# Kernel tuning notes

Hardware: AMD Instinct MI355X
Metric: run time of the kernel (lower is better)

The kernel has to match this reference:

```python
import jax, jax.numpy as jnp
import numpy as np

N, E = 50000, 600000
H, ED = 128, 64
LN_EPS = 1e-5


def _ln(x, g, b):
    mu = jnp.mean(x, axis=-1, keepdims=True)
    var = jnp.mean(jnp.square(x - mu), axis=-1, keepdims=True)
    return (x - mu) * jax.lax.rsqrt(var + LN_EPS) * g + b


def setup_inputs() -> dict:
    key = jax.random.key(0)
    ks = jax.random.split(key, 20)
    p = lambda k, shp: (jax.random.normal(k, shp, dtype=jnp.float32) * 0.02)
    return {
        "x": jax.random.normal(ks[0], (N, H), dtype=jnp.float32),
        "edge_src": jax.random.randint(ks[1], (E,), 0, N, dtype=jnp.int32),
        "edge_dst": jax.random.randint(ks[2], (E,), 0, N, dtype=jnp.int32),
        "edge_emb": jax.random.normal(ks[3], (E, ED), dtype=jnp.float32),
        "ln1_g": jnp.ones((H,), jnp.float32), "ln1_b": jnp.zeros((H,), jnp.float32),
        "W_self": p(ks[4], (H, H)), "b_self": jnp.zeros((H,), jnp.float32),
        "W_m1": p(ks[5], (H + ED, H)), "b_m1": jnp.zeros((H,), jnp.float32),
        "W_m2": p(ks[6], (H, H)), "b_m2": jnp.zeros((H,), jnp.float32),
        "W_g1": p(ks[7], (2 * H + ED, H)), "b_g1": jnp.zeros((H,), jnp.float32),
        "W_g2": p(ks[8], (H, 1)), "b_g2": jnp.zeros((1,), jnp.float32),
        "W_agg": p(ks[9], (H, H)), "b_agg": jnp.zeros((H,), jnp.float32),
        "ln2_g": jnp.ones((H,), jnp.float32), "ln2_b": jnp.zeros((H,), jnp.float32),
        "W_f1": p(ks[10], (H, 2 * H)), "b_f1": jnp.zeros((2 * H,), jnp.float32),
        "W_f2": p(ks[11], (2 * H, H)), "b_f2": jnp.zeros((H,), jnp.float32),
    }


def reference(x, edge_src, edge_dst, edge_emb,
              ln1_g, ln1_b, W_self, b_self,
              W_m1, b_m1, W_m2, b_m2,
              W_g1, b_g1, W_g2, b_g2,
              W_agg, b_agg, ln2_g, ln2_b,
              W_f1, b_f1, W_f2, b_f2):
    n = x.shape[0]
    h = _ln(x, ln1_g, ln1_b)                      # [N,H]
    hs = h[edge_src]                              # [E,H] gather
    hd = h[edge_dst]                              # [E,H] gather
    # message MLP on [h_src || e]
    m_in = jnp.concatenate([hs, edge_emb], axis=-1)            # [E,H+ED]
    msg = jax.nn.gelu(m_in @ W_m1 + b_m1, approximate=False) @ W_m2 + b_m2
    # gate MLP on [h_dst || h_src || e]
    g_in = jnp.concatenate([hd, hs, edge_emb], axis=-1)        # [E,2H+ED]
    gate = jax.nn.sigmoid(jax.nn.gelu(g_in @ W_g1 + b_g1, approximate=False) @ W_g2 + b_g2)
    edge_repr = gate * msg                                     # [E,H]
    # scatter-mean aggregate to destination nodes
    agg = jax.ops.segment_sum(edge_repr, edge_dst, num_segments=n)   # [N,H]
    deg = jax.ops.segment_sum(jnp.ones((edge_dst.shape[0], 1), x.dtype),
                              edge_dst, num_segments=n)              # [N,1]
    agg = agg / jnp.maximum(deg, 1.0)
    update = (h @ W_self + b_self) + (agg @ W_agg + b_agg)
    out = x + update                                           # residual
    ffn_in = _ln(out, ln2_g, ln2_b)
    ffn_up = jax.nn.gelu(ffn_in @ W_f1 + b_f1, approximate=False) @ W_f2 + b_f2
    out = out + ffn_up                                         # residual
    return (out, edge_repr)
```

## Files before the change

### kernel.cpp

```cpp
#include <hip/hip_runtime.h>
#include <math.h>

#define N_NODES 50000
#define N_EDGES 600000

typedef __attribute__((ext_vector_type(8))) short bf16x8;
typedef __attribute__((ext_vector_type(4))) float f32x4;

__device__ __forceinline__ unsigned short f2bf(float f){
  union { float f; unsigned int u; } v; v.f = f;
  unsigned int u = v.u;
  unsigned int r = (u + 0x7fffu + ((u >> 16) & 1u)) >> 16;
  return (unsigned short)r;
}
__device__ __forceinline__ float gelu_f(float x){
  return 0.5f * x * (1.0f + erff(x * 0.70710678118654752440f));
}

__global__ void pack_kernel(const float* __restrict__ W, unsigned short* __restrict__ out,
                            int K, int N){
  int id = blockIdx.x * 256 + threadIdx.x;
  if (id >= K * N) return;
  int j = id & 7;
  int q = (id >> 3) & 3;
  int rest = id >> 5;
  int n = rest % N;
  int kt = rest / N;
  int k = kt * 32 + q * 8 + j;
  out[id] = f2bf(W[(size_t)k * N + n]);
}

__global__ __launch_bounds__(256) void ln1_kernel(const float* __restrict__ x,
                                                  const float* __restrict__ g,
                                                  const float* __restrict__ b,
                                                  unsigned short* __restrict__ h_bf, int n){
  int row = blockIdx.x * 4 + (threadIdx.x >> 6);
  if (row >= n) return;
  int lane = threadIdx.x & 63;
  const float* xr = x + (size_t)row * 128;
  float2 v = *(const float2*)(xr + lane * 2);
  float s = v.x + v.y;
  float s2 = v.x * v.x + v.y * v.y;
#pragma unroll
  for (int off = 32; off; off >>= 1){ s += __shfl_xor(s, off); s2 += __shfl_xor(s2, off); }
  float mu = s * (1.f / 128.f);
  float var = s2 * (1.f / 128.f) - mu * mu;
  float rs = rsqrtf(var + 1e-5f);
  int c = lane * 2;
  ushort2 o;
  o.x = f2bf((v.x - mu) * rs * g[c] + b[c]);
  o.y = f2bf((v.y - mu) * rs * g[c + 1] + b[c + 1]);
  *(ushort2*)(h_bf + (size_t)row * 128 + c) = o;
}

__global__ __launch_bounds__(256, 2) void edge_kernel(
    const unsigned short* __restrict__ h_bf,
    const int* __restrict__ esrc, const int* __restrict__ edst,
    const float* __restrict__ emb,
    const unsigned short* __restrict__ Wm1p, const float* __restrict__ bm1,
    const unsigned short* __restrict__ Wm2p, const float* __restrict__ bm2,
    const unsigned short* __restrict__ Wg1p, const float* __restrict__ bg1,
    const float* __restrict__ wg2, const float* __restrict__ bg2,
    float* __restrict__ out_e, float* __restrict__ agg, float* __restrict__ deg)
{
  __shared__ unsigned short smA[64][328];
  __shared__ unsigned short smT[64][136];
  __shared__ float smGate[64];
  __shared__ int smDst[64];

  const int t = threadIdx.x;
  const int e0 = blockIdx.x * 64;

  if (t < 64){
    int d = edst[e0 + t];
    smDst[t] = d;
    atomicAdd(&deg[d], 1.0f);
  }
  {
    const int r = t >> 2, i = t & 3;
    const int e = e0 + r;
    const int ds = edst[e], ss = esrc[e];
    const uint4* hdp = (const uint4*)(h_bf + (size_t)ds * 128 + i * 32);
    const uint4* hsp = (const uint4*)(h_bf + (size_t)ss * 128 + i * 32);
    uint4* a0 = (uint4*)&smA[r][i * 32];
    uint4* a1 = (uint4*)&smA[r][128 + i * 32];
#pragma unroll
    for (int k2 = 0; k2 < 4; k2++){ a0[k2] = hdp[k2]; a1[k2] = hsp[k2]; }
    const float4* ep = (const float4*)(emb + (size_t)e * 64 + i * 16);
#pragma unroll
    for (int k2 = 0; k2 < 4; k2++){
      float4 f = ep[k2];
      ushort4 u; u.x = f2bf(f.x); u.y = f2bf(f.y); u.z = f2bf(f.z); u.w = f2bf(f.w);
      *(ushort4*)&smA[r][256 + i * 16 + k2 * 4] = u;
    }
  }
  __syncthreads();

  const int wave = t >> 6, lane = t & 63;
  const int q = lane >> 4, ln = lane & 15;
  const int arow = wave * 16 + ln;
  const int kq = q * 8;

  {
    f32x4 acc[8];
#pragma unroll
    for (int i = 0; i < 8; i++) acc[i] = (f32x4){0.f, 0.f, 0.f, 0.f};
#pragma unroll
    for (int kt = 0; kt < 10; kt++){
      bf16x8 a = *(const bf16x8*)&smA[arow][kt * 32 + kq];
#pragma unroll
      for (int nt = 0; nt < 8; nt++){
        bf16x8 b = *(const bf16x8*)(Wg1p + (((size_t)kt * 128 + nt * 16 + ln) * 4 + q) * 8);
        acc[nt] = __builtin_amdgcn_mfma_f32_16x16x32_bf16(a, b, acc[nt], 0, 0, 0);
      }
    }
    float p0 = 0.f, p1 = 0.f, p2 = 0.f, p3 = 0.f;
#pragma unroll
    for (int nt = 0; nt < 8; nt++){
      int col = nt * 16 + ln;
      float bia = bg1[col];
      float w2 = wg2[col];
      p0 += gelu_f(acc[nt][0] + bia) * w2;
      p1 += gelu_f(acc[nt][1] + bia) * w2;
      p2 += gelu_f(acc[nt][2] + bia) * w2;
      p3 += gelu_f(acc[nt][3] + bia) * w2;
    }
#pragma unroll
    for (int m = 1; m < 16; m <<= 1){
      p0 += __shfl_xor(p0, m); p1 += __shfl_xor(p1, m);
      p2 += __shfl_xor(p2, m); p3 += __shfl_xor(p3, m);
    }
    if (ln == 0){
      float bg = bg2[0];
      smGate[wave * 16 + q * 4 + 0] = 1.f / (1.f + expf(-(p0 + bg)));
      smGate[wave * 16 + q * 4 + 1] = 1.f / (1.f + expf(-(p1 + bg)));
      smGate[wave * 16 + q * 4 + 2] = 1.f / (1.f + expf(-(p2 + bg)));
      smGate[wave * 16 + q * 4 + 3] = 1.f / (1.f + expf(-(p3 + bg)));
    }
  }

  {
    f32x4 acc[8];
#pragma unroll
    for (int i = 0; i < 8; i++) acc[i] = (f32x4){0.f, 0.f, 0.f, 0.f};
#pragma unroll
    for (int kt = 0; kt < 6; kt++){
      bf16x8 a = *(const bf16x8*)&smA[arow][128 + kt * 32 + kq];
#pragma unroll
      for (int nt = 0; nt < 8; nt++){
        bf16x8 b = *(const bf16x8*)(Wm1p + (((size_t)kt * 128 + nt * 16 + ln) * 4 + q) * 8);
        acc[nt] = __builtin_amdgcn_mfma_f32_16x16x32_bf16(a, b, acc[nt], 0, 0, 0);
      }
    }
#pragma unroll
    for (int nt = 0; nt < 8; nt++){
      int col = nt * 16 + ln;
      float bia = bm1[col];
#pragma unroll
      for (int r = 0; r < 4; r++){
        smT[wave * 16 + q * 4 + r][col] = f2bf(gelu_f(acc[nt][r] + bia));
      }
    }
  }

  {
    f32x4 acc[8];
#pragma unroll
    for (int i = 0; i < 8; i++) acc[i] = (f32x4){0.f, 0.f, 0.f, 0.f};
#pragma unroll
    for (int kt = 0; kt < 4; kt++){
      bf16x8 a = *(const bf16x8*)&smT[arow][kt * 32 + kq];
#pragma unroll
      for (int nt = 0; nt < 8; nt++){
        bf16x8 b = *(const bf16x8*)(Wm2p + (((size_t)kt * 128 + nt * 16 + ln) * 4 + q) * 8);
        acc[nt] = __builtin_amdgcn_mfma_f32_16x16x32_bf16(a, b, acc[nt], 0, 0, 0);
      }
    }
#pragma unroll
    for (int nt = 0; nt < 8; nt++){
      int col = nt * 16 + ln;
      float bia = bm2[col];
#pragma unroll
      for (int r = 0; r < 4; r++){
        int row = wave * 16 + q * 4 + r;
        float val = smGate[row] * (acc[nt][r] + bia);
        out_e[(size_t)(e0 + row) * 128 + col] = val;
        atomicAdd(&agg[(size_t)smDst[row] * 128 + col], val);
      }
    }
  }
}

__global__ __launch_bounds__(256, 2) void node_kernel(
    const float* __restrict__ x, const unsigned short* __restrict__ h_bf,
    const float* __restrict__ agg, const float* __restrict__ deg,
    const unsigned short* __restrict__ Wselfp, const float* __restrict__ bself,
    const unsigned short* __restrict__ Waggp, const float* __restrict__ bagg,
    const float* __restrict__ ln2g, const float* __restrict__ ln2b,
    const unsigned short* __restrict__ Wf1p, const float* __restrict__ bf1,
    const unsigned short* __restrict__ Wf2p, const float* __restrict__ bf2,
    float* __restrict__ out, int n)
{
  __shared__ unsigned short smH[32][136];
  __shared__ unsigned short smG[32][136];
  __shared__ float smO[32][132];
  __shared__ unsigned short smU[32][264];

  const int t = threadIdx.x;
  const int n0 = blockIdx.x * 32;

  {
    const int r = t >> 3, i = t & 7;
    int gr = n0 + r; if (gr >= n) gr = n - 1;
    const uint4* hp = (const uint4*)(h_bf + (size_t)gr * 128 + i * 16);
    uint4* dp = (uint4*)&smH[r][i * 16];
    dp[0] = hp[0]; dp[1] = hp[1];
    float sc = 1.f / fmaxf(deg[gr], 1.f);
    const float4* ap = (const float4*)(agg + (size_t)gr * 128 + i * 16);
#pragma unroll
    for (int k2 = 0; k2 < 4; k2++){
      float4 f = ap[k2];
      ushort4 u; u.x = f2bf(f.x * sc); u.y = f2bf(f.y * sc); u.z = f2bf(f.z * sc); u.w = f2bf(f.w * sc);
      *(ushort4*)&smG[r][i * 16 + k2 * 4] = u;
    }
  }
  __syncthreads();

  const int wave = t >> 6, lane = t & 63;
  const int q = lane >> 4, ln = lane & 15;
  const int mtile = wave >> 1;
  const int cg = wave & 1;
  const int arow = mtile * 16 + ln;
  const int kq = q * 8;

  f32x4 acc[4];
#pragma unroll
  for (int i = 0; i < 4; i++) acc[i] = (f32x4){0.f, 0.f, 0.f, 0.f};
#pragma unroll
  for (int kt = 0; kt < 4; kt++){
    bf16x8 a = *(const bf16x8*)&smH[arow][kt * 32 + kq];
#pragma unroll
    for (int j = 0; j < 4; j++){
      int col = (cg * 4 + j) * 16 + ln;
      bf16x8 b = *(const bf16x8*)(Wselfp + (((size_t)kt * 128 + col) * 4 + q) * 8);
      acc[j] = __builtin_amdgcn_mfma_f32_16x16x32_bf16(a, b, acc[j], 0, 0, 0);
    }
  }
#pragma unroll
  for (int kt = 0; kt < 4; kt++){
    bf16x8 a = *(const bf16x8*)&smG[arow][kt * 32 + kq];
#pragma unroll
    for (int j = 0; j < 4; j++){
      int col = (cg * 4 + j) * 16 + ln;
      bf16x8 b = *(const bf16x8*)(Waggp + (((size_t)kt * 128 + col) * 4 + q) * 8);
      acc[j] = __builtin_amdgcn_mfma_f32_16x16x32_bf16(a, b, acc[j], 0, 0, 0);
    }
  }
#pragma unroll
  for (int j = 0; j < 4; j++){
    int col = (cg * 4 + j) * 16 + ln;
    float bia = bself[col] + bagg[col];
#pragma unroll
    for (int r = 0; r < 4; r++){
      int row = mtile * 16 + q * 4 + r;
      int gr = n0 + row; if (gr >= n) gr = n - 1;
      smO[row][col] = x[(size_t)gr * 128 + col] + acc[j][r] + bia;
    }
  }
  __syncthreads();

  {
    const int r = t >> 3, i = t & 7;
    float v[16];
    float s = 0.f, s2 = 0.f;
    const float4* op = (const float4*)&smO[r][i * 16];
#pragma unroll
    for (int k2 = 0; k2 < 4; k2++){
      float4 f = op[k2];
      v[k2 * 4 + 0] = f.x; v[k2 * 4 + 1] = f.y; v[k2 * 4 + 2] = f.z; v[k2 * 4 + 3] = f.w;
      s += f.x + f.y + f.z + f.w;
      s2 += f.x * f.x + f.y * f.y + f.z * f.z + f.w * f.w;
    }
#pragma unroll
    for (int m = 1; m < 8; m <<= 1){ s += __shfl_xor(s, m); s2 += __shfl_xor(s2, m); }
    float mu = s * (1.f / 128.f);
    float var = s2 * (1.f / 128.f) - mu * mu;
    float rs = rsqrtf(var + 1e-5f);
#pragma unroll
    for (int c2 = 0; c2 < 16; c2++){
      int col = i * 16 + c2;
      smH[r][col] = f2bf((v[c2] - mu) * rs * ln2g[col] + ln2b[col]);
    }
  }
  __syncthreads();

  {
    f32x4 au[8];
#pragma unroll
    for (int i = 0; i < 8; i++) au[i] = (f32x4){0.f, 0.f, 0.f, 0.f};
#pragma unroll
    for (int kt = 0; kt < 4; kt++){
      bf16x8 a = *(const bf16x8*)&smH[arow][kt * 32 + kq];
#pragma unroll
      for (int j = 0; j < 8; j++){
        int col = (cg * 8 + j) * 16 + ln;
        bf16x8 b = *(const bf16x8*)(Wf1p + (((size_t)kt * 256 + col) * 4 + q) * 8);
        au[j] = __builtin_amdgcn_mfma_f32_16x16x32_bf16(a, b, au[j], 0, 0, 0);
      }
    }
#pragma unroll
    for (int j = 0; j < 8; j++){
      int col = (cg * 8 + j) * 16 + ln;
      float bia = bf1[col];
#pragma unroll
      for (int r = 0; r < 4; r++){
        smU[mtile * 16 + q * 4 + r][col] = f2bf(gelu_f(au[j][r] + bia));
      }
    }
  }
  __syncthreads();

  {
    f32x4 a2[4];
#pragma unroll
    for (int i = 0; i < 4; i++) a2[i] = (f32x4){0.f, 0.f, 0.f, 0.f};
#pragma unroll
    for (int kt = 0; kt < 8; kt++){
      bf16x8 a = *(const bf16x8*)&smU[arow][kt * 32 + kq];
#pragma unroll
      for (int j = 0; j < 4; j++){
        int col = (cg * 4 + j) * 16 + ln;
        bf16x8 b = *(const bf16x8*)(Wf2p + (((size_t)kt * 128 + col) * 4 + q) * 8);
        a2[j] = __builtin_amdgcn_mfma_f32_16x16x32_bf16(a, b, a2[j], 0, 0, 0);
      }
    }
#pragma unroll
    for (int j = 0; j < 4; j++){
      int col = (cg * 4 + j) * 16 + ln;
      float bia = bf2[col];
#pragma unroll
      for (int r = 0; r < 4; r++){
        int row = mtile * 16 + q * 4 + r;
        int gr = n0 + row;
        if (gr < n) out[(size_t)gr * 128 + col] = smO[row][col] + a2[j][r] + bia;
      }
    }
  }
}

extern "C" void kernel_launch(void* const* d_in, const int* in_sizes, int n_in,
                              void* d_out, int out_size, void* d_ws, size_t ws_size,
                              hipStream_t stream){
  const float* x     = (const float*)d_in[0];
  const int*   esrc  = (const int*)d_in[1];
  const int*   edst  = (const int*)d_in[2];
  const float* eemb  = (const float*)d_in[3];
  const float* ln1g  = (const float*)d_in[4];
  const float* ln1b  = (const float*)d_in[5];
  const float* Wself = (const float*)d_in[6];
  const float* bself = (const float*)d_in[7];
  const float* Wm1   = (const float*)d_in[8];
  const float* bm1   = (const float*)d_in[9];
  const float* Wm2   = (const float*)d_in[10];
  const float* bm2   = (const float*)d_in[11];
  const float* Wg1   = (const float*)d_in[12];
  const float* bg1   = (const float*)d_in[13];
  const float* wg2   = (const float*)d_in[14];
  const float* bg2   = (const float*)d_in[15];
  const float* Wagg  = (const float*)d_in[16];
  const float* bagg  = (const float*)d_in[17];
  const float* ln2g  = (const float*)d_in[18];
  const float* ln2b  = (const float*)d_in[19];
  const float* Wf1   = (const float*)d_in[20];
  const float* bf1   = (const float*)d_in[21];
  const float* Wf2   = (const float*)d_in[22];
  const float* bf2   = (const float*)d_in[23];

  char* ws = (char*)d_ws;
  float* agg = (float*)(ws + 0);
  float* deg = (float*)(ws + 25600000);
  unsigned short* h_bf = (unsigned short*)(ws + 25800000);
  unsigned short* Wselfp = (unsigned short*)(ws + 38600000);
  unsigned short* Wm1p  = Wselfp + 16384;
  unsigned short* Wm2p  = Wm1p + 24576;
  unsigned short* Wg1p  = Wm2p + 16384;
  unsigned short* Waggp = Wg1p + 40960;
  unsigned short* Wf1p  = Waggp + 16384;
  unsigned short* Wf2p  = Wf1p + 32768;

  hipMemsetAsync(agg, 0, 25600000 + 200000, stream);

  pack_kernel<<<64, 256, 0, stream>>>(Wself, Wselfp, 128, 128);
  pack_kernel<<<96, 256, 0, stream>>>(Wm1, Wm1p, 192, 128);
  pack_kernel<<<64, 256, 0, stream>>>(Wm2, Wm2p, 128, 128);
  pack_kernel<<<160, 256, 0, stream>>>(Wg1, Wg1p, 320, 128);
  pack_kernel<<<64, 256, 0, stream>>>(Wagg, Waggp, 128, 128);
  pack_kernel<<<128, 256, 0, stream>>>(Wf1, Wf1p, 128, 256);
  pack_kernel<<<128, 256, 0, stream>>>(Wf2, Wf2p, 256, 128);

  ln1_kernel<<<12500, 256, 0, stream>>>(x, ln1g, ln1b, h_bf, N_NODES);

  float* out_nodes = (float*)d_out;
  float* out_edges = out_nodes + (size_t)N_NODES * 128;

  edge_kernel<<<N_EDGES / 64, 256, 0, stream>>>(h_bf, esrc, edst, eemb,
      Wm1p, bm1, Wm2p, bm2, Wg1p, bg1, wg2, bg2, out_edges, agg, deg);

  node_kernel<<<(N_NODES + 31) / 32, 256, 0, stream>>>(x, h_bf, agg, deg,
      Wselfp, bself, Waggp, bagg, ln2g, ln2b, Wf1p, bf1, Wf2p, bf2, out_nodes, N_NODES);
}
```

Measured before the change: 1.150 ms.

## Make edge kernel persistent with register-resident weight slices split by column

Turns the edge kernel into a persistent grid-stride loop over 64-edge tiles with 512 blocks. Each wave now owns a 32-column slice of every weight matrix, held in registers for the whole kernel, and computes all 64 rows against it, instead of re-reading all weights from global memory for every tile. The gate dot product becomes a cross-wave partial sum reduced through shared memory, which adds extra barriers. Keeping about 40 bf16x8 weight fragments per lane raises register pressure, which may cause spills or lower occupancy under launch_bounds(256,2).

```diff
diff --git a/kernel.cpp b/kernel.cpp
--- a/kernel.cpp
+++ b/kernel.cpp
@@ -3,6 +3,7 @@
 
 #define N_NODES 50000
 #define N_EDGES 600000
+#define NTILES (N_EDGES / 64)
 
 typedef __attribute__((ext_vector_type(8))) short bf16x8;
 typedef __attribute__((ext_vector_type(4))) float f32x4;
@@ -65,128 +66,158 @@
 {
   __shared__ unsigned short smA[64][328];
   __shared__ unsigned short smT[64][136];
+  __shared__ float smGP[4][64];
   __shared__ float smGate[64];
   __shared__ int smDst[64];
 
   const int t = threadIdx.x;
-  const int e0 = blockIdx.x * 64;
-
-  if (t < 64){
-    int d = edst[e0 + t];
-    smDst[t] = d;
-    atomicAdd(&deg[d], 1.0f);
-  }
-  {
-    const int r = t >> 2, i = t & 3;
-    const int e = e0 + r;
-    const int ds = edst[e], ss = esrc[e];
-    const uint4* hdp = (const uint4*)(h_bf + (size_t)ds * 128 + i * 32);
-    const uint4* hsp = (const uint4*)(h_bf + (size_t)ss * 128 + i * 32);
-    uint4* a0 = (uint4*)&smA[r][i * 32];
-    uint4* a1 = (uint4*)&smA[r][128 + i * 32];
-#pragma unroll
-    for (int k2 = 0; k2 < 4; k2++){ a0[k2] = hdp[k2]; a1[k2] = hsp[k2]; }
-    const float4* ep = (const float4*)(emb + (size_t)e * 64 + i * 16);
-#pragma unroll
-    for (int k2 = 0; k2 < 4; k2++){
-      float4 f = ep[k2];
-      ushort4 u; u.x = f2bf(f.x); u.y = f2bf(f.y); u.z = f2bf(f.z); u.w = f2bf(f.w);
-      *(ushort4*)&smA[r][256 + i * 16 + k2 * 4] = u;
-    }
-  }
-  __syncthreads();
-
   const int wave = t >> 6, lane = t & 63;
   const int q = lane >> 4, ln = lane & 15;
-  const int arow = wave * 16 + ln;
   const int kq = q * 8;
 
-  {
-    f32x4 acc[8];
-#pragma unroll
-    for (int i = 0; i < 8; i++) acc[i] = (f32x4){0.f, 0.f, 0.f, 0.f};
-#pragma unroll
-    for (int kt = 0; kt < 10; kt++){
-      bf16x8 a = *(const bf16x8*)&smA[arow][kt * 32 + kq];
-#pragma unroll
-      for (int nt = 0; nt < 8; nt++){
-        bf16x8 b = *(const bf16x8*)(Wg1p + (((size_t)kt * 128 + nt * 16 + ln) * 4 + q) * 8);
-        acc[nt] = __builtin_amdgcn_mfma_f32_16x16x32_bf16(a, b, acc[nt], 0, 0, 0);
-      }
-    }
-    float p0 = 0.f, p1 = 0.f, p2 = 0.f, p3 = 0.f;
-#pragma unroll
-    for (int nt = 0; nt < 8; nt++){
-      int col = nt * 16 + ln;
-      float bia = bg1[col];
-      float w2 = wg2[col];
-      p0 += gelu_f(acc[nt][0] + bia) * w2;
-      p1 += gelu_f(acc[nt][1] + bia) * w2;
-      p2 += gelu_f(acc[nt][2] + bia) * w2;
-      p3 += gelu_f(acc[nt][3] + bia) * w2;
-    }
-#pragma unroll
-    for (int m = 1; m < 16; m <<= 1){
-      p0 += __shfl_xor(p0, m); p1 += __shfl_xor(p1, m);
-      p2 += __shfl_xor(p2, m); p3 += __shfl_xor(p3, m);
-    }
-    if (ln == 0){
-      float bg = bg2[0];
-      smGate[wave * 16 + q * 4 + 0] = 1.f / (1.f + expf(-(p0 + bg)));
-      smGate[wave * 16 + q * 4 + 1] = 1.f / (1.f + expf(-(p1 + bg)));
-      smGate[wave * 16 + q * 4 + 2] = 1.f / (1.f + expf(-(p2 + bg)));
-      smGate[wave * 16 + q * 4 + 3] = 1.f / (1.f + expf(-(p3 + bg)));
-    }
-  }
-
-  {
-    f32x4 acc[8];
-#pragma unroll
-    for (int i = 0; i < 8; i++) acc[i] = (f32x4){0.f, 0.f, 0.f, 0.f};
-#pragma unroll
-    for (int kt = 0; kt < 6; kt++){
-      bf16x8 a = *(const bf16x8*)&smA[arow][128 + kt * 32 + kq];
-#pragma unroll
-      for (int nt = 0; nt < 8; nt++){
-        bf16x8 b = *(const bf16x8*)(Wm1p + (((size_t)kt * 128 + nt * 16 + ln) * 4 + q) * 8);
-        acc[nt] = __builtin_amdgcn_mfma_f32_16x16x32_bf16(a, b, acc[nt], 0, 0, 0);
-      }
-    }
-#pragma unroll
-    for (int nt = 0; nt < 8; nt++){
-      int col = nt * 16 + ln;
-      float bia = bm1[col];
-#pragma unroll
-      for (int r = 0; r < 4; r++){
-        smT[wave * 16 + q * 4 + r][col] = f2bf(gelu_f(acc[nt][r] + bia));
-      }
-    }
-  }
-
-  {
-    f32x4 acc[8];
-#pragma unroll
-    for (int i = 0; i < 8; i++) acc[i] = (f32x4){0.f, 0.f, 0.f, 0.f};
-#pragma unroll
-    for (int kt = 0; kt < 4; kt++){
-      bf16x8 a = *(const bf16x8*)&smT[arow][kt * 32 + kq];
-#pragma unroll
-      for (int nt = 0; nt < 8; nt++){
-        bf16x8 b = *(const bf16x8*)(Wm2p + (((size_t)kt * 128 + nt * 16 + ln) * 4 + q) * 8);
-        acc[nt] = __builtin_amdgcn_mfma_f32_16x16x32_bf16(a, b, acc[nt], 0, 0, 0);
-      }
-    }
-#pragma unroll
-    for (int nt = 0; nt < 8; nt++){
-      int col = nt * 16 + ln;
-      float bia = bm2[col];
-#pragma unroll
-      for (int r = 0; r < 4; r++){
-        int row = wave * 16 + q * 4 + r;
-        float val = smGate[row] * (acc[nt][r] + bia);
-        out_e[(size_t)(e0 + row) * 128 + col] = val;
-        atomicAdd(&agg[(size_t)smDst[row] * 128 + col], val);
-      }
+  bf16x8 wg[10][2], w1[6][2], w2[4][2];
+  float bg1r[2], wg2r[2], bm1r[2], bm2r[2];
+#pragma unroll
+  for (int j = 0; j < 2; j++){
+    const int col = wave * 32 + j * 16 + ln;
+    bg1r[j] = bg1[col]; wg2r[j] = wg2[col]; bm1r[j] = bm1[col]; bm2r[j] = bm2[col];
+#pragma unroll
+    for (int kt = 0; kt < 10; kt++) wg[kt][j] = *(const bf16x8*)(Wg1p + (((size_t)kt * 128 + col) * 4 + q) * 8);
+#pragma unroll
+    for (int kt = 0; kt < 6; kt++)  w1[kt][j] = *(const bf16x8*)(Wm1p + (((size_t)kt * 128 + col) * 4 + q) * 8);
+#pragma unroll
+    for (int kt = 0; kt < 4; kt++)  w2[kt][j] = *(const bf16x8*)(Wm2p + (((size_t)kt * 128 + col) * 4 + q) * 8);
+  }
+  const float bg2v = bg2[0];
+  const int r4 = t >> 2, i4 = t & 3;
+
+  for (int tile = blockIdx.x; tile < NTILES; tile += gridDim.x){
+    const int e0 = tile * 64;
+    __syncthreads();
+
+    {
+      const int e = e0 + r4;
+      const int ds = edst[e], ss = esrc[e];
+      if (i4 == 0){ smDst[r4] = ds; atomicAdd(&deg[ds], 1.0f); }
+      const uint4* hdp = (const uint4*)(h_bf + (size_t)ds * 128 + i4 * 32);
+      const uint4* hsp = (const uint4*)(h_bf + (size_t)ss * 128 + i4 * 32);
+      uint4* a0 = (uint4*)&smA[r4][i4 * 32];
+      uint4* a1 = (uint4*)&smA[r4][128 + i4 * 32];
+#pragma unroll
+      for (int k2 = 0; k2 < 4; k2++){ a0[k2] = hdp[k2]; a1[k2] = hsp[k2]; }
+      const float4* ep = (const float4*)(emb + (size_t)e * 64 + i4 * 16);
+#pragma unroll
+      for (int k2 = 0; k2 < 4; k2++){
+        float4 f = ep[k2];
+        ushort4 u; u.x = f2bf(f.x); u.y = f2bf(f.y); u.z = f2bf(f.z); u.w = f2bf(f.w);
+        *(ushort4*)&smA[r4][256 + i4 * 16 + k2 * 4] = u;
+      }
+    }
+    __syncthreads();
+
+    {
+      f32x4 acc[4][2];
+#pragma unroll
+      for (int rt = 0; rt < 4; rt++)
+#pragma unroll
+        for (int j = 0; j < 2; j++) acc[rt][j] = (f32x4){0.f, 0.f, 0.f, 0.f};
+#pragma unroll
+      for (int kt = 0; kt < 10; kt++){
+        bf16x8 a[4];
+#pragma unroll
+        for (int rt = 0; rt < 4; rt++) a[rt] = *(const bf16x8*)&smA[rt * 16 + ln][kt * 32 + kq];
+#pragma unroll
+        for (int rt = 0; rt < 4; rt++)
+#pragma unroll
+          for (int j = 0; j < 2; j++)
+            acc[rt][j] = __builtin_amdgcn_mfma_f32_16x16x32_bf16(a[rt], wg[kt][j], acc[rt][j], 0, 0, 0);
+      }
+      float p[4][4];
+#pragma unroll
+      for (int rt = 0; rt < 4; rt++)
+#pragma unroll
+        for (int r = 0; r < 4; r++)
+          p[rt][r] = gelu_f(acc[rt][0][r] + bg1r[0]) * wg2r[0]
+                   + gelu_f(acc[rt][1][r] + bg1r[1]) * wg2r[1];
+#pragma unroll
+      for (int m = 1; m < 16; m <<= 1){
+#pragma unroll
+        for (int rt = 0; rt < 4; rt++)
+#pragma unroll
+          for (int r = 0; r < 4; r++) p[rt][r] += __shfl_xor(p[rt][r], m);
+      }
+      if (ln == 0){
+#pragma unroll
+        for (int rt = 0; rt < 4; rt++)
+#pragma unroll
+          for (int r = 0; r < 4; r++) smGP[wave][rt * 16 + q * 4 + r] = p[rt][r];
+      }
+    }
+    __syncthreads();
+    if (t < 64)
+      smGate[t] = 1.f / (1.f + expf(-(smGP[0][t] + smGP[1][t] + smGP[2][t] + smGP[3][t] + bg2v)));
+
+    {
+      f32x4 acc[4][2];
+#pragma unroll
+      for (int rt = 0; rt < 4; rt++)
+#pragma unroll
+        for (int j = 0; j < 2; j++) acc[rt][j] = (f32x4){0.f, 0.f, 0.f, 0.f};
+#pragma unroll
+      for (int kt = 0; kt < 6; kt++){
+        bf16x8 a[4];
+#pragma unroll
+        for (int rt = 0; rt < 4; rt++) a[rt] = *(const bf16x8*)&smA[rt * 16 + ln][128 + kt * 32 + kq];
+#pragma unroll
+        for (int rt = 0; rt < 4; rt++)
+#pragma unroll
+          for (int j = 0; j < 2; j++)
+            acc[rt][j] = __builtin_amdgcn_mfma_f32_16x16x32_bf16(a[rt], w1[kt][j], acc[rt][j], 0, 0, 0);
+      }
+#pragma unroll
+      for (int rt = 0; rt < 4; rt++)
+#pragma unroll
+        for (int j = 0; j < 2; j++){
+          const int col = wave * 32 + j * 16 + ln;
+          const float bia = bm1r[j];
+#pragma unroll
+          for (int r = 0; r < 4; r++)
+            smT[rt * 16 + q * 4 + r][col] = f2bf(gelu_f(acc[rt][j][r] + bia));
+        }
+    }
+    __syncthreads();
+
+    {
+      f32x4 acc[4][2];
+#pragma unroll
+      for (int rt = 0; rt < 4; rt++)
+#pragma unroll
+        for (int j = 0; j < 2; j++) acc[rt][j] = (f32x4){0.f, 0.f, 0.f, 0.f};
+#pragma unroll
+      for (int kt = 0; kt < 4; kt++){
+        bf16x8 a[4];
+#pragma unroll
+        for (int rt = 0; rt < 4; rt++) a[rt] = *(const bf16x8*)&smT[rt * 16 + ln][kt * 32 + kq];
+#pragma unroll
+        for (int rt = 0; rt < 4; rt++)
+#pragma unroll
+          for (int j = 0; j < 2; j++)
+            acc[rt][j] = __builtin_amdgcn_mfma_f32_16x16x32_bf16(a[rt], w2[kt][j], acc[rt][j], 0, 0, 0);
+      }
+#pragma unroll
+      for (int rt = 0; rt < 4; rt++)
+#pragma unroll
+        for (int j = 0; j < 2; j++){
+          const int col = wave * 32 + j * 16 + ln;
+          const float bia = bm2r[j];
+#pragma unroll
+          for (int r = 0; r < 4; r++){
+            const int row = rt * 16 + q * 4 + r;
+            const float val = smGate[row] * (acc[rt][j][r] + bia);
+            out_e[(size_t)(e0 + row) * 128 + col] = val;
+            atomicAdd(&agg[(size_t)smDst[row] * 128 + col], val);
+          }
+        }
     }
   }
 }
@@ -403,7 +434,7 @@
   float* out_nodes = (float*)d_out;
   float* out_edges = out_nodes + (size_t)N_NODES * 128;
 
-  edge_kernel<<<N_EDGES / 64, 256, 0, stream>>>(h_bf, esrc, edst, eemb,
+  edge_kernel<<<512, 256, 0, stream>>>(h_bf, esrc, edst, eemb,
       Wm1p, bm1, Wm2p, bm2, Wg1p, bg1, wg2, bg2, out_edges, agg, deg);
 
   node_kernel<<<(N_NODES + 31) / 32, 256, 0, stream>>>(x, h_bf, agg, deg,
```

New measurement: 953.8 us. 17.0% less time.
